# Performance work log

Hardware: AMD Instinct MI355X
Metric: run time of the kernel (lower is better)

## Reference

```python
import jax, jax.numpy as jnp
import numpy as np

B, S, D, H = 4, 2048, 1024, 16
DH = D // H


def setup_inputs() -> dict:
    key = jax.random.key(0)
    k1, k2, k3 = jax.random.split(key, 3)
    x = jax.random.normal(k1, (B, S, D), dtype=jnp.float32)
    w_attn = jax.random.normal(k2, (D, 3 * D), dtype=jnp.float32) * 0.02
    b_attn = jnp.zeros((3 * D,), dtype=jnp.float32)
    w_proj = jax.random.normal(k3, (D, D), dtype=jnp.float32) * 0.02
    b_proj = jnp.zeros((D,), dtype=jnp.float32)
    return {"x": x, "w_attn": w_attn, "b_attn": b_attn, "w_proj": w_proj, "b_proj": b_proj}


def _split_heads(t):
    # [B, S, D] -> [B, H, S, DH]
    return t.reshape(B, S, H, DH).transpose(0, 2, 1, 3)


def reference(x, w_attn, b_attn, w_proj, b_proj):
    # fused QKV projection (TFConv1D = x @ w + b)
    qkv = jnp.einsum('bsd,df->bsf', x, w_attn) + b_attn  # [B, S, 3D]
    q, k, v = jnp.split(qkv, 3, axis=2)
    q, k, v = _split_heads(q), _split_heads(k), _split_heads(v)  # [B,H,S,DH]

    # scaled scores
    w = jnp.einsum('bhqd,bhkd->bhqk', q, k) / jnp.sqrt(jnp.asarray(DH, dtype=q.dtype))

    # causal mask: multiply + additive -10000 trick, as in original
    i = jnp.arange(S)[:, None]
    j = jnp.arange(S)[None, :]
    b = (i >= j).astype(w.dtype)  # nd == ns so i >= j - ns + nd == i >= j
    b = b[None, None]  # [1,1,S,S]
    w = w * b - 10000.0 * (1.0 - b)

    w = jax.nn.softmax(w, axis=-1)
    # attn_pdrop = 0.0 -> dropout is identity (eval)

    a = jnp.einsum('bhqk,bhkd->bhqd', w, v)  # [B,H,S,DH]
    a = a.transpose(0, 2, 1, 3).reshape(B, S, D)  # merge heads
    a = jnp.einsum('bsd,df->bsf', a, w_proj) + b_proj
    # resid_pdrop = 0.0 -> identity
    return a
```

## Files before the change

kernel.cpp:

```cpp
#include <hip/hip_runtime.h>
#include <stdint.h>

typedef __bf16 bf16x8 __attribute__((ext_vector_type(8)));
typedef float  f32x4  __attribute__((ext_vector_type(4)));

#define DEV __device__ __forceinline__

constexpr int Bc = 4, S = 2048, D = 1024, Hh = 16, DH = 64;
constexpr int Kdim = 1024;

DEV unsigned short f2bf(float f) {
    uint32_t u = __builtin_bit_cast(uint32_t, f);
    u += 0x7fff + ((u >> 16) & 1);
    return (unsigned short)(u >> 16);
}
DEV bf16x8 ld8(const unsigned short* p) {
    uint4 u = *(const uint4*)p;
    return __builtin_bit_cast(bf16x8, u);
}
DEV uint4 pack8(float4 a, float4 b) {
    union { uint4 u; unsigned short s[8]; } r;
    r.s[0] = f2bf(a.x); r.s[1] = f2bf(a.y); r.s[2] = f2bf(a.z); r.s[3] = f2bf(a.w);
    r.s[4] = f2bf(b.x); r.s[5] = f2bf(b.y); r.s[6] = f2bf(b.z); r.s[7] = f2bf(b.w);
    return r.u;
}

DEV void gl16(const void* g, void* l) {
    __builtin_amdgcn_global_load_lds((__attribute__((address_space(1))) void*)g,
                                     (__attribute__((address_space(3))) void*)l,
                                     16, 0, 0);
}

__global__ __launch_bounds__(256) void transpose_cvt(const float* __restrict__ in,
                                                     unsigned short* __restrict__ out,
                                                     int rows, int cols) {
    __shared__ float t[32][33];
    int tx = threadIdx.x & 31, ty = threadIdx.x >> 5;
    int c = blockIdx.x * 32 + tx;
    int rbase = blockIdx.y * 32;
    for (int rr = 0; rr < 32; rr += 8)
        t[ty + rr][tx] = in[(size_t)(rbase + ty + rr) * cols + c];
    __syncthreads();
    int orbase = blockIdx.x * 32;
    for (int rr = 0; rr < 32; rr += 8)
        out[(size_t)(orbase + ty + rr) * rows + rbase + tx] = f2bf(t[tx][ty + rr]);
}

__global__ __launch_bounds__(256) void cvt_bf16(const float* __restrict__ in,
                                                unsigned short* __restrict__ out) {
    size_t i = (size_t)blockIdx.x * 256 + threadIdx.x;
    const float4* p = (const float4*)(in + i * 8);
    float4 a = p[0], b = p[1];
    *(uint4*)(out + i * 8) = pack8(a, b);
}

__global__ __launch_bounds__(256) void gemm_bt(const unsigned short* __restrict__ A,
                                               const unsigned short* __restrict__ Bt,
                                               const float* __restrict__ bias,
                                               int mode,
                                               unsigned short* __restrict__ qo,
                                               unsigned short* __restrict__ ko,
                                               unsigned short* __restrict__ vo,
                                               float* __restrict__ outf) {
    __shared__ __align__(16) unsigned short As[128 * 32];
    __shared__ __align__(16) unsigned short Bs[128 * 32];
    const int tid = threadIdx.x;
    const int wave = tid >> 6, lane = tid & 63, g = lane >> 4, ln = lane & 15;
    const int wm = wave >> 1, wn = wave & 1;
    const int m0 = blockIdx.y * 128, n0 = blockIdx.x * 128;

    f32x4 acc[4][4];
    for (int i = 0; i < 4; i++)
        for (int j = 0; j < 4; j++) acc[i][j] = f32x4{0.f, 0.f, 0.f, 0.f};

    for (int k0 = 0; k0 < Kdim; k0 += 32) {
#pragma unroll
        for (int c = 0; c < 2; c++) {
            int L = c * 4096 + tid * 16;
            int row = L >> 6, colb = L & 63;
            gl16((const char*)A  + ((size_t)(m0 + row) * Kdim + k0) * 2 + colb,
                 (char*)As + c * 4096 + wave * 1024);
            gl16((const char*)Bt + ((size_t)(n0 + row) * Kdim + k0) * 2 + colb,
                 (char*)Bs + c * 4096 + wave * 1024);
        }
        __syncthreads();
        bf16x8 af[4], bfr[4];
        for (int t = 0; t < 4; t++) af[t]  = ld8(As + (wm * 64 + t * 16 + ln) * 32 + g * 8);
        for (int t = 0; t < 4; t++) bfr[t] = ld8(Bs + (wn * 64 + t * 16 + ln) * 32 + g * 8);
        for (int mt = 0; mt < 4; mt++)
            for (int nt = 0; nt < 4; nt++)
                acc[mt][nt] = __builtin_amdgcn_mfma_f32_16x16x32_bf16(af[mt], bfr[nt], acc[mt][nt], 0, 0, 0);
        __syncthreads();
    }

    for (int mt = 0; mt < 4; mt++)
        for (int nt = 0; nt < 4; nt++)
            for (int r = 0; r < 4; r++) {
                int m = m0 + wm * 64 + mt * 16 + g * 4 + r;
                int n = n0 + wn * 64 + nt * 16 + ln;
                float val = acc[mt][nt][r] + bias[n];
                if (mode == 0) {
                    int which = n >> 10, rem = n & 1023;
                    int hh = rem >> 6, dd = rem & 63;
                    int b = m >> 11, s = m & 2047;
                    int bh = (b << 4) + hh;
                    if (which == 0)      qo[((size_t)bh * S + s) * DH + dd] = f2bf(val);
                    else if (which == 1) ko[((size_t)bh * S + s) * DH + dd] = f2bf(val);
                    else                 vo[((size_t)bh * DH + dd) * S + s] = f2bf(val);
                } else {
                    outf[(size_t)m * 1024 + n] = val;
                }
            }
}

__global__ __launch_bounds__(256, 3) void attn_fwd(const unsigned short* __restrict__ qg,
                                                   const unsigned short* __restrict__ kg,
                                                   const unsigned short* __restrict__ vtg,
                                                   unsigned short* __restrict__ og) {
    __shared__ __align__(16) unsigned short Ks[128 * 64];
    __shared__ __align__(16) unsigned short Vs[64 * 128];
    __shared__ __align__(16) unsigned short P [64 * 136];
    const int idx = blockIdx.x;
    const int qt = 31 - (idx >> 6);
    const int bh = idx & 63;
    const int b = bh >> 4, h = bh & 15;
    const size_t base = (size_t)bh * S * DH;
    const unsigned short* qp = qg + base;
    const char* kpb  = (const char*)(kg  + base);
    const char* vtpb = (const char*)(vtg + base);
    const int tid = threadIdx.x, wave = tid >> 6, lane = tid & 63;
    const int g = lane >> 4, ln = lane & 15;
    const int q0 = qt * 64, wq = wave * 16;
    const int jn = (qt >> 1) + 1;

    bf16x8 qf[2];
    qf[0] = ld8(qp + (size_t)(q0 + wq + ln) * DH + g * 8);
    qf[1] = ld8(qp + (size_t)(q0 + wq + ln) * DH + 32 + g * 8);

    f32x4 o_t[4];
#pragma unroll
    for (int dt = 0; dt < 4; dt++) o_t[dt] = f32x4{0.f, 0.f, 0.f, 0.f};
    float m_ = -1e30f, l_ = 0.f;

#pragma unroll 1
    for (int j = 0; j < jn; j++) {
        const char* kj = kpb + (size_t)j * (128 * DH * 2);
        const char* vj = vtpb + j * 256;
#pragma unroll
        for (int c = 0; c < 4; c++) {
            int L = c * 4096 + tid * 16;
            int kr = L >> 7, kcb = L & 127;
            gl16(kj + (size_t)kr * 128 + (kcb ^ ((kr & 7) << 4)),
                 (char*)Ks + c * 4096 + wave * 1024);
            int vr = L >> 8, vcb = L & 255;
            gl16(vj + (size_t)vr * 4096 + (vcb ^ ((vr & 15) << 4)),
                 (char*)Vs + c * 4096 + wave * 1024);
        }
        __syncthreads();

        f32x4 st[8];
#pragma unroll
        for (int mt = 0; mt < 8; mt++) {
            int row = mt * 16 + ln;
            int sw = (row & 7) << 4;
            const char* kb2 = (const char*)Ks + row * 128;
            bf16x8 kf0 = ld8((const unsigned short*)(kb2 + ((g * 16) ^ sw)));
            bf16x8 kf1 = ld8((const unsigned short*)(kb2 + ((64 + g * 16) ^ sw)));
            f32x4 t = f32x4{0.f, 0.f, 0.f, 0.f};
            t = __builtin_amdgcn_mfma_f32_16x16x32_bf16(kf0, qf[0], t, 0, 0, 0);
            t = __builtin_amdgcn_mfma_f32_16x16x32_bf16(kf1, qf[1], t, 0, 0, 0);
            st[mt] = t;
        }
        if (j == jn - 1) {
            int qgl = q0 + wq + ln;
#pragma unroll
            for (int mt = 0; mt < 8; mt++)
#pragma unroll
                for (int r = 0; r < 4; r++) {
                    int kvg = j * 128 + mt * 16 + g * 4 + r;
                    if (kvg > qgl) st[mt][r] = -3e38f;
                }
        }
        f32x4 mm = st[0];
#pragma unroll
        for (int mt = 1; mt < 8; mt++)
#pragma unroll
            for (int e = 0; e < 4; e++) mm[e] = fmaxf(mm[e], st[mt][e]);
        float mx = fmaxf(fmaxf(mm[0], mm[1]), fmaxf(mm[2], mm[3]));
        mx = fmaxf(mx, __shfl_xor(mx, 16));
        mx = fmaxf(mx, __shfl_xor(mx, 32));
        float mnew = fmaxf(m_, mx);
        float alpha = __expf((m_ - mnew) * 0.125f);
        f32x4 sv = f32x4{0.f, 0.f, 0.f, 0.f};
#pragma unroll
        for (int mt = 0; mt < 8; mt++) {
            f32x4 pr;
#pragma unroll
            for (int e = 0; e < 4; e++) pr[e] = __expf((st[mt][e] - mnew) * 0.125f);
            st[mt] = pr;
            sv += pr;
        }
        float rs = (sv[0] + sv[1]) + (sv[2] + sv[3]);
        rs += __shfl_xor(rs, 16);
        rs += __shfl_xor(rs, 32);
        l_ = l_ * alpha + rs;
        m_ = mnew;

#pragma unroll
        for (int mt = 0; mt < 8; mt++) {
            uint4 u = __builtin_bit_cast(uint4, st[mt]);
            uint2 w;
            w.x = (u.y & 0xFFFF0000u) | (u.x >> 16);
            w.y = (u.w & 0xFFFF0000u) | (u.z >> 16);
            *(uint2*)&P[(wq + ln) * 136 + mt * 16 + g * 4] = w;
        }
#pragma unroll
        for (int dt = 0; dt < 4; dt++) o_t[dt] *= alpha;

#pragma unroll
        for (int kc = 0; kc < 4; kc++) {
            bf16x8 pf = ld8(&P[(wq + ln) * 136 + kc * 32 + g * 8]);
            bf16x8 vf[4];
#pragma unroll
            for (int dt = 0; dt < 4; dt++) {
                int row = dt * 16 + ln;
                vf[dt] = ld8((const unsigned short*)((const char*)Vs + row * 256 +
                             ((kc * 64 + g * 16) ^ ((row & 15) << 4))));
            }
#pragma unroll
            for (int dt = 0; dt < 4; dt++)
                o_t[dt] = __builtin_amdgcn_mfma_f32_16x16x32_bf16(vf[dt], pf, o_t[dt], 0, 0, 0);
        }
        __syncthreads();
    }

    float il = 1.f / l_;
#pragma unroll
    for (int dt = 0; dt < 4; dt++) o_t[dt] *= il;
    float* Ot = (float*)&P[wq * 136];
#pragma unroll
    for (int dt = 0; dt < 4; dt++)
        *(float4*)&Ot[ln * 68 + dt * 16 + g * 4] =
            float4{o_t[dt][0], o_t[dt][1], o_t[dt][2], o_t[dt][3]};
#pragma unroll
    for (int i = 0; i < 4; i++) {
        float4 v = *(float4*)&Ot[(i * 4 + g) * 68 + ln * 4];
        uint2 w;
        w.x = (uint32_t)f2bf(v.x) | ((uint32_t)f2bf(v.y) << 16);
        w.y = (uint32_t)f2bf(v.z) | ((uint32_t)f2bf(v.w) << 16);
        *(uint2*)&og[((size_t)(b * S + q0 + wq + i * 4 + g)) * D + h * DH + ln * 4] = w;
    }
}

extern "C" void kernel_launch(void* const* d_in, const int* in_sizes, int n_in,
                              void* d_out, int out_size, void* d_ws, size_t ws_size,
                              hipStream_t stream) {
    (void)in_sizes; (void)n_in; (void)out_size; (void)ws_size;
    const float* x      = (const float*)d_in[0];
    const float* w_attn = (const float*)d_in[1];
    const float* b_attn = (const float*)d_in[2];
    const float* w_proj = (const float*)d_in[3];
    const float* b_proj = (const float*)d_in[4];

    char* ws = (char*)d_ws;
    unsigned short* wattn_t = (unsigned short*)ws;
    unsigned short* wproj_t = (unsigned short*)(ws + 6291456);
    unsigned short* xb      = (unsigned short*)(ws + 8388608);
    unsigned short* qb      = (unsigned short*)(ws + 25165824);
    unsigned short* kb      = (unsigned short*)(ws + 41943040);
    unsigned short* vtb     = (unsigned short*)(ws + 58720256);
    unsigned short* aob     = (unsigned short*)(ws + 75497472);

    transpose_cvt<<<dim3(96, 32), 256, 0, stream>>>(w_attn, wattn_t, 1024, 3072);
    transpose_cvt<<<dim3(32, 32), 256, 0, stream>>>(w_proj, wproj_t, 1024, 1024);
    cvt_bf16<<<dim3(4096), 256, 0, stream>>>(x, xb);
    gemm_bt<<<dim3(24, 64), 256, 0, stream>>>(xb, wattn_t, b_attn, 0, qb, kb, vtb, nullptr);
    attn_fwd<<<dim3(2048), 256, 0, stream>>>(qb, kb, vtb, aob);
    gemm_bt<<<dim3(8, 64), 256, 0, stream>>>(aob, wproj_t, b_proj, 1,
                                             nullptr, nullptr, nullptr, (float*)d_out);
}
```

Measured before the change: 285.5 us.

## Double-buffer GEMM loads, prefetch K/V in attention, stage QKV epilogue via LDS

The GEMM now double-buffers its A/B tiles in shared memory, issuing the next k-slice's async global-to-LDS loads before computing the current one, with vmcnt waits and raw barriers in place of __syncthreads. The attention kernel splits the K and V staging so the next block's K load overlaps softmax and the next V load overlaps the end of the PV step. The QKV epilogue writes through LDS so the global stores become 16-byte contiguous (including the transposed V), replacing scattered 2-byte stores. This adds more LDS in the GEMM and relies on hand-counted vmcnt values, which could race if the count of outstanding loads is off.

```diff
diff --git a/kernel.cpp b/kernel.cpp
--- a/kernel.cpp
+++ b/kernel.cpp
@@ -54,16 +54,15 @@
     *(uint4*)(out + i * 8) = pack8(a, b);
 }
 
-__global__ __launch_bounds__(256) void gemm_bt(const unsigned short* __restrict__ A,
-                                               const unsigned short* __restrict__ Bt,
-                                               const float* __restrict__ bias,
-                                               int mode,
-                                               unsigned short* __restrict__ qo,
-                                               unsigned short* __restrict__ ko,
-                                               unsigned short* __restrict__ vo,
-                                               float* __restrict__ outf) {
-    __shared__ __align__(16) unsigned short As[128 * 32];
-    __shared__ __align__(16) unsigned short Bs[128 * 32];
+__global__ __launch_bounds__(256, 5) void gemm_bt(const unsigned short* __restrict__ A,
+                                                  const unsigned short* __restrict__ Bt,
+                                                  const float* __restrict__ bias,
+                                                  int mode,
+                                                  unsigned short* __restrict__ qo,
+                                                  unsigned short* __restrict__ ko,
+                                                  unsigned short* __restrict__ vo,
+                                                  float* __restrict__ outf) {
+    __shared__ __align__(16) unsigned short sh[4][4096];
     const int tid = threadIdx.x;
     const int wave = tid >> 6, lane = tid & 63, g = lane >> 4, ln = lane & 15;
     const int wm = wave >> 1, wn = wave & 1;
@@ -73,44 +72,91 @@
     for (int i = 0; i < 4; i++)
         for (int j = 0; j < 4; j++) acc[i][j] = f32x4{0.f, 0.f, 0.f, 0.f};
 
+#define STAGE_G(buf, k0)                                                            \
+    _Pragma("unroll")                                                               \
+    for (int c = 0; c < 2; c++) {                                                   \
+        int L = c * 4096 + tid * 16;                                                \
+        int row = L >> 6, colb = L & 63;                                            \
+        gl16((const char*)A  + ((size_t)(m0 + row) * Kdim + (k0)) * 2 + colb,       \
+             (char*)sh[buf]     + c * 4096 + wave * 1024);                          \
+        gl16((const char*)Bt + ((size_t)(n0 + row) * Kdim + (k0)) * 2 + colb,       \
+             (char*)sh[2 + (buf)] + c * 4096 + wave * 1024);                        \
+    }
+
+    STAGE_G(0, 0);
+#pragma unroll 2
     for (int k0 = 0; k0 < Kdim; k0 += 32) {
-#pragma unroll
-        for (int c = 0; c < 2; c++) {
-            int L = c * 4096 + tid * 16;
-            int row = L >> 6, colb = L & 63;
-            gl16((const char*)A  + ((size_t)(m0 + row) * Kdim + k0) * 2 + colb,
-                 (char*)As + c * 4096 + wave * 1024);
-            gl16((const char*)Bt + ((size_t)(n0 + row) * Kdim + k0) * 2 + colb,
-                 (char*)Bs + c * 4096 + wave * 1024);
-        }
-        __syncthreads();
+        const int buf = (k0 >> 5) & 1;
+        if (k0 + 32 < Kdim) {
+            STAGE_G(buf ^ 1, k0 + 32);
+            asm volatile("s_waitcnt vmcnt(4)" ::: "memory");
+        } else {
+            asm volatile("s_waitcnt vmcnt(0)" ::: "memory");
+        }
+        __builtin_amdgcn_s_barrier();
+        const unsigned short* As = sh[buf];
+        const unsigned short* Bs = sh[2 + buf];
         bf16x8 af[4], bfr[4];
         for (int t = 0; t < 4; t++) af[t]  = ld8(As + (wm * 64 + t * 16 + ln) * 32 + g * 8);
         for (int t = 0; t < 4; t++) bfr[t] = ld8(Bs + (wn * 64 + t * 16 + ln) * 32 + g * 8);
         for (int mt = 0; mt < 4; mt++)
             for (int nt = 0; nt < 4; nt++)
                 acc[mt][nt] = __builtin_amdgcn_mfma_f32_16x16x32_bf16(af[mt], bfr[nt], acc[mt][nt], 0, 0, 0);
+        __builtin_amdgcn_s_barrier();
+        asm volatile("" ::: "memory");
+    }
+#undef STAGE_G
+
+    if (mode == 0) {
+        unsigned short* E = &sh[0][0];
+        const int which = n0 >> 10;
+        const int hh0 = (n0 & 1023) >> 6;
+        const int b = m0 >> 11;
+        const int s0 = m0 & 2047;
+#pragma unroll
+        for (int nt = 0; nt < 4; nt++) {
+            float bv = bias[n0 + wn * 64 + nt * 16 + ln];
+#pragma unroll
+            for (int mt = 0; mt < 4; mt++)
+#pragma unroll
+                for (int r = 0; r < 4; r++) {
+                    int ml = wm * 64 + mt * 16 + g * 4 + r;
+                    int nl = wn * 64 + nt * 16 + ln;
+                    unsigned short v = f2bf(acc[mt][nt][r] + bv);
+                    if (which == 2) E[nl * 128 + ml] = v;
+                    else            E[ml * 128 + nl] = v;
+                }
+        }
         __syncthreads();
-    }
-
-    for (int mt = 0; mt < 4; mt++)
-        for (int nt = 0; nt < 4; nt++)
-            for (int r = 0; r < 4; r++) {
-                int m = m0 + wm * 64 + mt * 16 + g * 4 + r;
-                int n = n0 + wn * 64 + nt * 16 + ln;
-                float val = acc[mt][nt][r] + bias[n];
-                if (mode == 0) {
-                    int which = n >> 10, rem = n & 1023;
-                    int hh = rem >> 6, dd = rem & 63;
-                    int b = m >> 11, s = m & 2047;
-                    int bh = (b << 4) + hh;
-                    if (which == 0)      qo[((size_t)bh * S + s) * DH + dd] = f2bf(val);
-                    else if (which == 1) ko[((size_t)bh * S + s) * DH + dd] = f2bf(val);
-                    else                 vo[((size_t)bh * DH + dd) * S + s] = f2bf(val);
-                } else {
-                    outf[(size_t)m * 1024 + n] = val;
+        if (which == 2) {
+#pragma unroll
+            for (int t = 0; t < 8; t++) {
+                int e = (t * 256 + tid) * 8;
+                int nl = e >> 7, mlo = e & 127;
+                int dd = nl & 63, hh = hh0 + (nl >> 6);
+                size_t dst = ((size_t)((b * 16 + hh) * 64 + dd)) * 2048 + s0 + mlo;
+                *(uint4*)(vo + dst) = *(const uint4*)(E + e);
+            }
+        } else {
+            unsigned short* qk = which ? ko : qo;
+#pragma unroll
+            for (int t = 0; t < 8; t++) {
+                int e = (t * 256 + tid) * 8;
+                int ml = e >> 7, nn = e & 127;
+                int dd = nn & 63, hh = hh0 + (nn >> 6);
+                size_t dst = ((size_t)((b * 16 + hh) * 2048 + s0 + ml)) * 64 + dd;
+                *(uint4*)(qk + dst) = *(const uint4*)(E + e);
+            }
+        }
+    } else {
+        for (int mt = 0; mt < 4; mt++)
+            for (int nt = 0; nt < 4; nt++)
+                for (int r = 0; r < 4; r++) {
+                    int m = m0 + wm * 64 + mt * 16 + g * 4 + r;
+                    int n = n0 + wn * 64 + nt * 16 + ln;
+                    outf[(size_t)m * 1024 + n] = acc[mt][nt][r] + bias[n];
                 }
-            }
+    }
 }
 
 __global__ __launch_bounds__(256, 3) void attn_fwd(const unsigned short* __restrict__ qg,
@@ -137,6 +183,30 @@
     qf[0] = ld8(qp + (size_t)(q0 + wq + ln) * DH + g * 8);
     qf[1] = ld8(qp + (size_t)(q0 + wq + ln) * DH + 32 + g * 8);
 
+#define STAGE_K(j)                                                                  \
+    {   const char* kj = kpb + (size_t)(j) * (128 * DH * 2);                        \
+        _Pragma("unroll")                                                           \
+        for (int c = 0; c < 4; c++) {                                               \
+            int L = c * 4096 + tid * 16;                                            \
+            int kr = L >> 7, kcb = L & 127;                                         \
+            gl16(kj + (size_t)kr * 128 + (kcb ^ ((kr & 7) << 4)),                   \
+                 (char*)Ks + c * 4096 + wave * 1024);                               \
+        }                                                                           \
+    }
+#define STAGE_V(j)                                                                  \
+    {   const char* vj = vtpb + (j) * 256;                                          \
+        _Pragma("unroll")                                                           \
+        for (int c = 0; c < 4; c++) {                                               \
+            int L = c * 4096 + tid * 16;                                            \
+            int vr = L >> 8, vcb = L & 255;                                         \
+            gl16(vj + (size_t)vr * 4096 + (vcb ^ ((vr & 15) << 4)),                 \
+                 (char*)Vs + c * 4096 + wave * 1024);                               \
+        }                                                                           \
+    }
+
+    STAGE_K(0);
+    STAGE_V(0);
+
     f32x4 o_t[4];
 #pragma unroll
     for (int dt = 0; dt < 4; dt++) o_t[dt] = f32x4{0.f, 0.f, 0.f, 0.f};
@@ -144,19 +214,8 @@
 
 #pragma unroll 1
     for (int j = 0; j < jn; j++) {
-        const char* kj = kpb + (size_t)j * (128 * DH * 2);
-        const char* vj = vtpb + j * 256;
-#pragma unroll
-        for (int c = 0; c < 4; c++) {
-            int L = c * 4096 + tid * 16;
-            int kr = L >> 7, kcb = L & 127;
-            gl16(kj + (size_t)kr * 128 + (kcb ^ ((kr & 7) << 4)),
-                 (char*)Ks + c * 4096 + wave * 1024);
-            int vr = L >> 8, vcb = L & 255;
-            gl16(vj + (size_t)vr * 4096 + (vcb ^ ((vr & 15) << 4)),
-                 (char*)Vs + c * 4096 + wave * 1024);
-        }
-        __syncthreads();
+        asm volatile("s_waitcnt vmcnt(4)" ::: "memory");
+        __builtin_amdgcn_s_barrier();
 
         f32x4 st[8];
 #pragma unroll
@@ -171,6 +230,10 @@
             t = __builtin_amdgcn_mfma_f32_16x16x32_bf16(kf1, qf[1], t, 0, 0, 0);
             st[mt] = t;
         }
+        __builtin_amdgcn_s_barrier();
+        asm volatile("" ::: "memory");
+        if (j + 1 < jn) STAGE_K(j + 1);
+
         if (j == jn - 1) {
             int qgl = q0 + wq + ln;
 #pragma unroll
@@ -217,6 +280,10 @@
 #pragma unroll
         for (int dt = 0; dt < 4; dt++) o_t[dt] *= alpha;
 
+        if (j + 1 < jn) asm volatile("s_waitcnt vmcnt(4)" ::: "memory");
+        else            asm volatile("s_waitcnt vmcnt(0)" ::: "memory");
+        __builtin_amdgcn_s_barrier();
+
 #pragma unroll
         for (int kc = 0; kc < 4; kc++) {
             bf16x8 pf = ld8(&P[(wq + ln) * 136 + kc * 32 + g * 8]);
@@ -231,8 +298,12 @@
             for (int dt = 0; dt < 4; dt++)
                 o_t[dt] = __builtin_amdgcn_mfma_f32_16x16x32_bf16(vf[dt], pf, o_t[dt], 0, 0, 0);
         }
-        __syncthreads();
-    }
+        __builtin_amdgcn_s_barrier();
+        asm volatile("" ::: "memory");
+        if (j + 1 < jn) STAGE_V(j + 1);
+    }
+#undef STAGE_K
+#undef STAGE_V
 
     float il = 1.f / l_;
 #pragma unroll
```

Measured after the change: 343.6 us. +20.4%, slower.
